# Kernel optimization log

Measured on AMD Instinct MI355X. Metric: run time of the kernel, lower is better.

The kernel has to match this reference:

```python
import jax, jax.numpy as jnp
import numpy as np

ALPHA = 0.95       # synaptic decay for layers l>0
BETA = 0.9         # membrane decay
THRESHOLD = 1.0
RESET = 0.0        # reset_potential
SIM_T = 100        # simulation_time
SG_SCALE = 100.0   # SuperSpike surrogate-gradient scale (SurrGradSpike)

@jax.custom_vjp
def spike(x):
    # forward: Heaviside step on (mem - threshold)
    return (x > 0).astype(x.dtype)

def _spike_fwd(x):
    return spike(x), x

def _spike_bwd(x, g):
    # SuperSpike surrogate: grad / (scale*|x| + 1)^2
    return (g / (SG_SCALE * jnp.abs(x) + 1.0) ** 2,)

spike.defvjp(_spike_fwd, _spike_bwd)


def setup_inputs() -> dict:
    key = jax.random.key(0)
    k1, k2, k3 = jax.random.split(key, 3)
    B, D, H = 256, 1024, 2048
    inputs = jax.random.normal(k1, (B, D), dtype=jnp.float32)
    w0 = jax.random.normal(k2, (D, H), dtype=jnp.float32) / np.sqrt(D).astype(np.float32)
    w1 = jax.random.normal(k3, (H, H), dtype=jnp.float32) / np.sqrt(H).astype(np.float32)
    return {"inputs": inputs, "w0": w0, "w1": w1}


def _simulate(inputs, w0, w1):
    B = inputs.shape[0]
    H0, H1 = w0.shape[1], w1.shape[1]
    # torch code does inputs.detach().clone() each step -> no grad to inputs
    x = jax.lax.stop_gradient(inputs)

    def step(carry, _):
        s0, m0, s1, m1 = carry
        # layer 0: new_syn = 0*syn + input @ W0
        ns0 = x @ w0
        nm0 = BETA * m0 + ns0
        mthr = nm0 - THRESHOLD          # hidden (non-final) layer spikes
        z = spike(mthr)
        nm0 = jnp.where(mthr > 0, RESET, nm0)   # masked reset after spike
        # layer 1 (final, non-spiking readout): new_syn = alpha*syn + z @ W1
        ns1 = ALPHA * s1 + z @ w1
        nm1 = BETA * m1 + ns1
        return (ns0, nm0, ns1, nm1), (nm0, nm1, z)

    init = (jnp.zeros((B, H0), jnp.float32), jnp.zeros((B, H0), jnp.float32),
            jnp.zeros((B, H1), jnp.float32), jnp.zeros((B, H1), jnp.float32))
    # torch loop records zeros at t==0 and updates for t=1..T-1
    _, (mem0_rec, mem1_rec, spk_rec) = jax.lax.scan(step, init, None, length=SIM_T - 1)
    z0 = jnp.zeros((1, B, H0), jnp.float32)
    z1 = jnp.zeros((1, B, H1), jnp.float32)
    mem0_rec = jnp.concatenate([z0, mem0_rec], axis=0)   # [T, B, H0]
    mem1_rec = jnp.concatenate([z1, mem1_rec], axis=0)   # [T, B, H1]
    spk_rec = jnp.concatenate([z0, spk_rec], axis=0)     # [T, B, H0]
    mem_rec = jnp.stack([mem0_rec, mem1_rec], axis=1)    # [T, L=2, B, H]
    return mem1_rec[-1], mem_rec, spk_rec


def reference(inputs, w0, w1):
    # returns (mem_rec[-1][-1], mem_rec, spk_rec) like the torch module
    return _simulate(inputs, w0, w1)
```

## Files before the change

### kernel.cpp

```cpp
#include <hip/hip_runtime.h>
#include <hip/hip_bf16.h>

#define Bdim 256
#define Ddim 1024
#define Hdim 2048
#define Tdim 100
#define BH (Bdim*Hdim)
#define M3 ((Tdim-1)*Bdim)
#define ZB8 ((size_t)M3*Hdim)

#define OUT_MEM ((size_t)BH)
#define OUT_SPK ((size_t)BH + (size_t)Tdim*2*BH)

typedef __attribute__((ext_vector_type(8))) short short8;
typedef __attribute__((ext_vector_type(4))) float f32x4;
typedef __attribute__((ext_vector_type(4))) int   i32x4;

#define GLD16(g, l) __builtin_amdgcn_global_load_lds( \
    (__attribute__((address_space(1))) void*)(g), \
    (__attribute__((address_space(3))) void*)(l), 16, 0, 0)

#define BARL() do { asm volatile("" ::: "memory"); __builtin_amdgcn_s_barrier(); \
                    asm volatile("" ::: "memory"); } while(0)

static __device__ __forceinline__ unsigned short bf16bits(float f) {
  __hip_bfloat16 h = __float2bfloat16(f);
  return *reinterpret_cast<unsigned short*>(&h);
}

__global__ __launch_bounds__(256) void kcvt_split(const float* __restrict__ X,
                                                  unsigned short* __restrict__ Xhi,
                                                  unsigned short* __restrict__ Xlo) {
  int i = (blockIdx.x*256 + threadIdx.x)*4;
  float4 v = *reinterpret_cast<const float4*>(&X[i]);
  ushort4 ph, pl;
  float f, fh;
  f = v.x; { __hip_bfloat16 h = __float2bfloat16(f); fh = __bfloat162float(h); ph.x = *reinterpret_cast<unsigned short*>(&h); } pl.x = bf16bits(f - fh);
  f = v.y; { __hip_bfloat16 h = __float2bfloat16(f); fh = __bfloat162float(h); ph.y = *reinterpret_cast<unsigned short*>(&h); } pl.y = bf16bits(f - fh);
  f = v.z; { __hip_bfloat16 h = __float2bfloat16(f); fh = __bfloat162float(h); ph.z = *reinterpret_cast<unsigned short*>(&h); } pl.z = bf16bits(f - fh);
  f = v.w; { __hip_bfloat16 h = __float2bfloat16(f); fh = __bfloat162float(h); ph.w = *reinterpret_cast<unsigned short*>(&h); } pl.w = bf16bits(f - fh);
  *reinterpret_cast<ushort4*>(&Xhi[i]) = ph;
  *reinterpret_cast<ushort4*>(&Xlo[i]) = pl;
}

__global__ __launch_bounds__(256) void ktr_split(const float* __restrict__ In,
                                                 unsigned short* __restrict__ OutHi,
                                                 unsigned short* __restrict__ OutLo,
                                                 int R, int C) {
  __shared__ unsigned short thi[32][33];
  __shared__ unsigned short tlo[32][33];
  int bk = blockIdx.x*32, bn = blockIdx.y*32;
  int tx = threadIdx.x & 31, ty = threadIdx.x >> 5;
  for (int r = ty; r < 32; r += 8) {
    float f = In[(size_t)(bk + r)*C + bn + tx];
    __hip_bfloat16 h = __float2bfloat16(f);
    float fh = __bfloat162float(h);
    thi[r][tx] = *reinterpret_cast<unsigned short*>(&h);
    tlo[r][tx] = bf16bits(f - fh);
  }
  __syncthreads();
  for (int r = ty; r < 32; r += 8) {
    OutHi[(size_t)(bn + r)*R + bk + tx] = thi[tx][r];
    OutLo[(size_t)(bn + r)*R + bk + tx] = tlo[tx][r];
  }
}

__global__ __launch_bounds__(256) void kcolmax_part(const float* __restrict__ W1,
                                                    float* __restrict__ pmax) {
  int n = blockIdx.x*256 + threadIdx.x;
  int kc = blockIdx.y;
  float m = 0.f;
  #pragma unroll 8
  for (int k = kc*64; k < kc*64 + 64; ++k)
    m = fmaxf(m, fabsf(W1[(size_t)k*Hdim + n]));
  pmax[(size_t)kc*Hdim + n] = m;
}

__global__ __launch_bounds__(256) void kcolmax_fin(const float* __restrict__ pmax,
                                                   float* __restrict__ scales) {
  int n = blockIdx.x*256 + threadIdx.x;
  float m = 0.f;
  #pragma unroll
  for (int i = 0; i < 32; ++i)
    m = fmaxf(m, pmax[(size_t)i*Hdim + n]);
  scales[n] = m * (1.0f/127.0f);
}

__global__ __launch_bounds__(256) void ktr_i8(const float* __restrict__ In,
                                              const float* __restrict__ scales,
                                              signed char* __restrict__ Out) {
  __shared__ signed char tile[32][33];
  int bk = blockIdx.x*32, bn = blockIdx.y*32;
  int tx = threadIdx.x & 31, ty = threadIdx.x >> 5;
  float rs = 1.0f / scales[bn + tx];
  for (int r = ty; r < 32; r += 8)
    tile[r][tx] = (signed char)(int)rintf(In[(size_t)(bk + r)*Hdim + bn + tx] * rs);
  __syncthreads();
  for (int r = ty; r < 32; r += 8)
    Out[(size_t)(bn + r)*Hdim + bk + tx] = tile[tx][r];
}

#define K1F_NK 32
__global__ __launch_bounds__(256) void k1_fused(const unsigned short* __restrict__ xhi,
                                                const unsigned short* __restrict__ xlo,
                                                const unsigned short* __restrict__ whiT,
                                                const unsigned short* __restrict__ wloT,
                                                float* __restrict__ NS0) {
  __shared__ short Ah[2][64*32], Al[2][64*32];
  __shared__ short Bh[2][64*32], Bl[2][64*32];
  int tid = threadIdx.x;
  int l = tid & 63, w = tid >> 6;
  int wm = w >> 1, wn = w & 1;
  int lr = l & 15, lg = l >> 4;
  size_t gm = (size_t)blockIdx.x * 64;
  size_t gn = (size_t)blockIdx.y * 64;
  int srow = l >> 2;
  int scol = ((l & 3)*8) ^ (((l >> 2) & 6) << 2);
  const unsigned short* gah = &xhi [(gm + w*16 + srow)*1024 + scol];
  const unsigned short* gal = &xlo [(gm + w*16 + srow)*1024 + scol];
  const unsigned short* gbh = &whiT[(gn + w*16 + srow)*1024 + scol];
  const unsigned short* gbl = &wloT[(gn + w*16 + srow)*1024 + scol];
  int rdswz = (lr & 6) << 2;
  f32x4 acc[2][2] = {};
  GLD16(gah, &Ah[0][w*512]); GLD16(gal, &Al[0][w*512]);
  GLD16(gbh, &Bh[0][w*512]); GLD16(gbl, &Bl[0][w*512]);
  __syncthreads();
  #pragma unroll 2
  for (int t = 0; t < K1F_NK; ++t) {
    int cur = t & 1;
    if (t + 1 < K1F_NK) {
      int nxt = cur ^ 1; size_t ko = (size_t)(t + 1)*32;
      GLD16(gah + ko, &Ah[nxt][w*512]); GLD16(gal + ko, &Al[nxt][w*512]);
      GLD16(gbh + ko, &Bh[nxt][w*512]); GLD16(gbl + ko, &Bl[nxt][w*512]);
    }
    short8 ah[2], al[2], bh[2], bl[2];
    #pragma unroll
    for (int mi = 0; mi < 2; ++mi) {
      int ro = (wm*32 + mi*16 + lr)*32 + (lg*8 ^ rdswz);
      ah[mi] = *reinterpret_cast<const short8*>(&Ah[cur][ro]);
      al[mi] = *reinterpret_cast<const short8*>(&Al[cur][ro]);
    }
    #pragma unroll
    for (int ni = 0; ni < 2; ++ni) {
      int ro = (wn*32 + ni*16 + lr)*32 + (lg*8 ^ rdswz);
      bh[ni] = *reinterpret_cast<const short8*>(&Bh[cur][ro]);
      bl[ni] = *reinterpret_cast<const short8*>(&Bl[cur][ro]);
    }
    #pragma unroll
    for (int mi = 0; mi < 2; ++mi)
      #pragma unroll
      for (int ni = 0; ni < 2; ++ni) {
        acc[mi][ni] = __builtin_amdgcn_mfma_f32_16x16x32_bf16(ah[mi], bh[ni], acc[mi][ni], 0, 0, 0);
        acc[mi][ni] = __builtin_amdgcn_mfma_f32_16x16x32_bf16(ah[mi], bl[ni], acc[mi][ni], 0, 0, 0);
        acc[mi][ni] = __builtin_amdgcn_mfma_f32_16x16x32_bf16(al[mi], bh[ni], acc[mi][ni], 0, 0, 0);
      }
    __syncthreads();
  }
  #pragma unroll
  for (int mi = 0; mi < 2; ++mi)
    #pragma unroll
    for (int ni = 0; ni < 2; ++ni)
      #pragma unroll
      for (int q = 0; q < 4; ++q)
        NS0[(gm + wm*32 + mi*16 + lg*4 + q)*Hdim + gn + wn*32 + ni*16 + lr] = acc[mi][ni][q];
}

__global__ __launch_bounds__(256) void k2_sim(const float* __restrict__ NS0,
                                              float* __restrict__ out,
                                              signed char* __restrict__ Zb) {
  size_t i4 = ((size_t)blockIdx.x*256 + threadIdx.x)*4;
  float4 nsv = *reinterpret_cast<const float4*>(&NS0[i4]);
  float ns[4] = {nsv.x, nsv.y, nsv.z, nsv.w};
  float* mem = out + OUT_MEM;
  float* spk = out + OUT_SPK;
  float4 z4 = {0.f, 0.f, 0.f, 0.f};
  *reinterpret_cast<float4*>(&mem[i4]) = z4;
  *reinterpret_cast<float4*>(&mem[BH + i4]) = z4;
  *reinterpret_cast<float4*>(&spk[i4]) = z4;
  float m[4] = {0.f, 0.f, 0.f, 0.f};
  for (int t = 1; t < Tdim; ++t) {
    float4 mo, zf; uchar4 z8;
    #pragma unroll
    for (int j = 0; j < 4; ++j) {
      m[j] = __fadd_rn(__fmul_rn(0.9f, m[j]), ns[j]);
      bool sp = m[j] > 1.0f;
      if (sp) m[j] = 0.f;
      ((float*)&mo)[j] = m[j];
      ((float*)&zf)[j] = sp ? 1.f : 0.f;
      ((unsigned char*)&z8)[j] = sp ? (unsigned char)1 : (unsigned char)0;
    }
    *reinterpret_cast<float4*>(&mem[(size_t)(2*t)*BH + i4]) = mo;
    *reinterpret_cast<float4*>(&spk[(size_t)t*BH + i4]) = zf;
    *reinterpret_cast<uchar4*>(&Zb[(size_t)(t-1)*BH + i4]) = z8;
  }
}

#define NKT3 32

#define K3_ST(g, ldsarr, half, kt) \
  GLD16((g) + (size_t)(kt)*64 + (size_t)(half)*128*2048, &ldsarr[(kt)&1][(half)*8192 + w*1024])

#define K3_LDA(h) do { \
  _Pragma("unroll") \
  for (int mi = 0; mi < 4; ++mi) \
    af[mi] = *reinterpret_cast<const i32x4*>( \
      &As[bb][((h)*128 + wm*64 + mi*16 + lr)*64 + ((lg ^ rxa)<<4)]); \
} while(0)

#define K3_LDB(v, bf) do { \
  _Pragma("unroll") \
  for (int ni = 0; ni < 2; ++ni) \
    bf[ni] = *reinterpret_cast<const i32x4*>( \
      &Bs[bb][((v)*128 + wn*32 + ni*16 + lr)*64 + ((lg ^ rxa)<<4)]); \
} while(0)

#define K3_MFMA(h, v, bf) do { \
  __builtin_amdgcn_s_setprio(1); \
  _Pragma("unroll") \
  for (int mi = 0; mi < 4; ++mi) \
    _Pragma("unroll") \
    for (int ni = 0; ni < 2; ++ni) \
      acc[(h)*4+mi][(v)*2+ni] = __builtin_amdgcn_mfma_i32_16x16x64_i8(af[mi], bf[ni], acc[(h)*4+mi][(v)*2+ni], 0, 0, 0); \
  __builtin_amdgcn_s_setprio(0); \
} while(0)

template<int CB>
__global__ __launch_bounds__(512, 2) void k3_gemm(const signed char* __restrict__ A,
                                                  const signed char* __restrict__ BT,
                                                  const float* __restrict__ scales,
                                                  float* __restrict__ mem1,
                                                  unsigned short* __restrict__ cbuf) {
  __shared__ signed char As[2][256*64];
  __shared__ signed char Bs[2][256*64];
  int tid = threadIdx.x;
  int l = tid & 63;
  int w = tid >> 6;
  int wm = w >> 2, wn = w & 3;
  int lr = l & 15, lg = l >> 4;
  int rxa = (lr >> 1) & 3;

  int lin = blockIdx.x;
  int wg = (lin & 7)*99 + (lin >> 3);
  int mtile = wg >> 3, ntile = wg & 7;
  size_t gm = (size_t)mtile * 256;
  size_t gn = (size_t)ntile * 256;

  int srow = l >> 2;
  int scol = ((l & 3) ^ ((l >> 3) & 3)) << 4;
  const signed char* gA = &A [(gm + w*16 + srow)*2048 + scol];
  const signed char* gB = &BT[(gn + w*16 + srow)*2048 + scol];

  i32x4 acc[8][4] = {};

  K3_ST(gA, As, 0, 0); K3_ST(gB, Bs, 0, 0);
  K3_ST(gA, As, 1, 0); K3_ST(gB, Bs, 1, 0);
  K3_ST(gA, As, 0, 1); K3_ST(gB, Bs, 1, 1);

  for (int kt = 0; kt < NKT3; ++kt) {
    int bb = kt & 1;
    if (kt == NKT3 - 1) asm volatile("s_waitcnt vmcnt(0)" ::: "memory");
    else                asm volatile("s_waitcnt vmcnt(2)" ::: "memory");
    __builtin_amdgcn_s_barrier();
    asm volatile("" ::: "memory");

    i32x4 af[4], bfl[2], bfh[2];

    K3_LDA(0); K3_LDB(0, bfl);
    if (kt + 1 < NKT3) K3_ST(gA, As, 1, kt + 1);
    BARL();
    K3_MFMA(0, 0, bfl);
    BARL();
    K3_LDB(1, bfh);
    if (kt + 1 < NKT3) K3_ST(gB, Bs, 0, kt + 1);
    BARL();
    K3_MFMA(0, 1, bfh);
    BARL();
    K3_LDA(1);
    if (kt + 2 < NKT3) K3_ST(gA, As, 0, kt + 2);
    BARL();
    K3_MFMA(1, 1, bfh);
    BARL();
    if (kt + 2 < NKT3) K3_ST(gB, Bs, 1, kt + 2);
    K3_MFMA(1, 0, bfl);
  }

  float sc[2][2];
  #pragma unroll
  for (int vv = 0; vv < 2; ++vv)
    #pragma unroll
    for (int ni = 0; ni < 2; ++ni)
      sc[vv][ni] = scales[gn + vv*128 + wn*32 + ni*16 + lr];

  if (CB) {
    unsigned short* cp = cbuf + (size_t)mtile*BH + gn;
    #pragma unroll
    for (int hh = 0; hh < 2; ++hh)
      #pragma unroll
      for (int mi = 0; mi < 4; ++mi)
        #pragma unroll
        for (int vv = 0; vv < 2; ++vv)
          #pragma unroll
          for (int ni = 0; ni < 2; ++ni)
            #pragma unroll
            for (int q = 0; q < 4; ++q) {
              int b   = hh*128 + wm*64 + mi*16 + lg*4 + q;
              int col = vv*128 + wn*32 + ni*16 + lr;
              cp[(size_t)b*Hdim + col] =
                bf16bits((float)acc[hh*4+mi][vv*2+ni][q] * sc[vv][ni]);
            }
  } else {
    float* plane = mem1 + (size_t)(2*mtile + 3)*BH + gn;
    #pragma unroll
    for (int hh = 0; hh < 2; ++hh)
      #pragma unroll
      for (int mi = 0; mi < 4; ++mi)
        #pragma unroll
        for (int vv = 0; vv < 2; ++vv)
          #pragma unroll
          for (int ni = 0; ni < 2; ++ni)
            #pragma unroll
            for (int q = 0; q < 4; ++q) {
              int b   = hh*128 + wm*64 + mi*16 + lg*4 + q;
              int col = vv*128 + wn*32 + ni*16 + lr;
              plane[(size_t)b*Hdim + col] =
                (float)acc[hh*4+mi][vv*2+ni][q] * sc[vv][ni];
            }
  }
}

__global__ __launch_bounds__(256) void k4_rec(float* __restrict__ out) {
  size_t i4 = ((size_t)blockIdx.x*256 + threadIdx.x)*4;
  float* mem = out + OUT_MEM;
  float s[4] = {0.f,0.f,0.f,0.f}, m[4] = {0.f,0.f,0.f,0.f};
  for (int t = 1; t < Tdim; ++t) {
    float4* p = reinterpret_cast<float4*>(&mem[(size_t)(2*t + 1)*BH + i4]);
    float4 c = *p;
    float4 mo;
    #pragma unroll
    for (int j = 0; j < 4; ++j) {
      s[j] = __fadd_rn(__fmul_rn(0.95f, s[j]), ((float*)&c)[j]);
      m[j] = __fadd_rn(__fmul_rn(0.9f, m[j]), s[j]);
      ((float*)&mo)[j] = m[j];
    }
    *p = mo;
  }
  float4 o = {m[0], m[1], m[2], m[3]};
  *reinterpret_cast<float4*>(&out[i4]) = o;
}

__global__ __launch_bounds__(256) void k4_rec_cb(const unsigned short* __restrict__ C,
                                                 float* __restrict__ out) {
  size_t i4 = ((size_t)blockIdx.x*256 + threadIdx.x)*4;
  float* mem = out + OUT_MEM;
  float s[4] = {0.f,0.f,0.f,0.f}, m[4] = {0.f,0.f,0.f,0.f};
  for (int t = 1; t < Tdim; ++t) {
    ushort4 cv = *reinterpret_cast<const ushort4*>(&C[(size_t)(t-1)*BH + i4]);
    float4 mo;
    #pragma unroll
    for (int j = 0; j < 4; ++j) {
      unsigned int u = ((unsigned short*)&cv)[j];
      float c = __uint_as_float(u << 16);
      s[j] = __fadd_rn(__fmul_rn(0.95f, s[j]), c);
      m[j] = __fadd_rn(__fmul_rn(0.9f, m[j]), s[j]);
      ((float*)&mo)[j] = m[j];
    }
    *reinterpret_cast<float4*>(&mem[(size_t)(2*t + 1)*BH + i4]) = mo;
  }
  float4 o = {m[0], m[1], m[2], m[3]};
  *reinterpret_cast<float4*>(&out[i4]) = o;
}

extern "C" void kernel_launch(void* const* d_in, const int* in_sizes, int n_in,
                              void* d_out, int out_size, void* d_ws, size_t ws_size,
                              hipStream_t stream) {
  const float* X  = (const float*)d_in[0];
  const float* W0 = (const float*)d_in[1];
  const float* W1 = (const float*)d_in[2];
  float* out = (float*)d_out;
  char* ws = (char*)d_ws;

  float*          ns0    = (float*)ws;
  signed char*    w1t8   = (signed char*)(ws + (2ull << 20));
  float*          scales = (float*)(ws + (6ull << 20));
  float*          pmax   = (float*)(ws + (6ull << 20) + (64ull << 10));
  signed char*    zb     = (signed char*)(ws + (10ull << 20));
  unsigned short* cbuf   = (unsigned short*)(ws + (10ull << 20) + ZB8);
  size_t needCb = (10ull << 20) + ZB8 + (size_t)M3*Hdim*2;
  int useCb = (ws_size >= needCb) ? 1 : 0;
  unsigned short* xhi = (unsigned short*)(ws + (10ull << 20));
  unsigned short* xlo = (unsigned short*)(ws + (10ull << 20) + (512<<10));
  unsigned short* whi = (unsigned short*)(ws + (11ull << 20));
  unsigned short* wlo = (unsigned short*)(ws + (15ull << 20));

  kcvt_split  <<<dim3(256),     256, 0, stream>>>(X, xhi, xlo);
  ktr_split   <<<dim3(32, 64),  256, 0, stream>>>(W0, whi, wlo, 1024, 2048);
  kcolmax_part<<<dim3(8, 32),   256, 0, stream>>>(W1, pmax);
  kcolmax_fin <<<dim3(8),       256, 0, stream>>>(pmax, scales);
  ktr_i8      <<<dim3(64, 64),  256, 0, stream>>>(W1, scales, w1t8);
  k1_fused    <<<dim3(4, 32),   256, 0, stream>>>(xhi, xlo, whi, wlo, ns0);
  k2_sim      <<<dim3(BH/1024), 256, 0, stream>>>(ns0, out, zb);
  if (useCb) {
    k3_gemm<1><<<dim3((M3/256)*(Hdim/256)), 512, 0, stream>>>(zb, w1t8, scales, out + OUT_MEM, cbuf);
    k4_rec_cb<<<dim3(BH/1024), 256, 0, stream>>>(cbuf, out);
  } else {
    k3_gemm<0><<<dim3((M3/256)*(Hdim/256)), 512, 0, stream>>>(zb, w1t8, scales, out + OUT_MEM, cbuf);
    k4_rec  <<<dim3(BH/1024), 256, 0, stream>>>(out);
  }
}
```

Baseline: 377.2 us.

## Simplify int8 GEMM main loop to whole-tile double buffering with one barrier

Replaces the staggered half-tile prefetch schedule in the int8 GEMM, which put a barrier around each MFMA quarter, with a plain double-buffered loop. Each iteration now issues all global-to-LDS loads for the next K tile, runs the four MFMA groups on the current tile, then waits for the loads and synchronises once. This cuts barrier count and scheduling constraints per K step. In exchange, loads are issued only one tile ahead and are drained fully before every barrier, so memory latency may be hidden less well.

```diff
diff --git a/kernel.cpp b/kernel.cpp
--- a/kernel.cpp
+++ b/kernel.cpp
@@ -19,9 +19,6 @@
 #define GLD16(g, l) __builtin_amdgcn_global_load_lds( \
     (__attribute__((address_space(1))) void*)(g), \
     (__attribute__((address_space(3))) void*)(l), 16, 0, 0)
-
-#define BARL() do { asm volatile("" ::: "memory"); __builtin_amdgcn_s_barrier(); \
-                    asm volatile("" ::: "memory"); } while(0)
 
 static __device__ __forceinline__ unsigned short bf16bits(float f) {
   __hip_bfloat16 h = __float2bfloat16(f);
@@ -252,36 +249,28 @@
 
   i32x4 acc[8][4] = {};
 
-  K3_ST(gA, As, 0, 0); K3_ST(gB, Bs, 0, 0);
-  K3_ST(gA, As, 1, 0); K3_ST(gB, Bs, 1, 0);
-  K3_ST(gA, As, 0, 1); K3_ST(gB, Bs, 1, 1);
+  K3_ST(gA, As, 0, 0); K3_ST(gA, As, 1, 0);
+  K3_ST(gB, Bs, 0, 0); K3_ST(gB, Bs, 1, 0);
+  asm volatile("s_waitcnt vmcnt(0)" ::: "memory");
+  __builtin_amdgcn_s_barrier();
+  asm volatile("" ::: "memory");
 
   for (int kt = 0; kt < NKT3; ++kt) {
     int bb = kt & 1;
-    if (kt == NKT3 - 1) asm volatile("s_waitcnt vmcnt(0)" ::: "memory");
-    else                asm volatile("s_waitcnt vmcnt(2)" ::: "memory");
+    if (kt + 1 < NKT3) {
+      K3_ST(gA, As, 0, kt + 1); K3_ST(gA, As, 1, kt + 1);
+      K3_ST(gB, Bs, 0, kt + 1); K3_ST(gB, Bs, 1, kt + 1);
+    }
+    i32x4 af[4], bfl[2], bfh[2];
+    K3_LDA(0); K3_LDB(0, bfl); K3_LDB(1, bfh);
+    K3_MFMA(0, 0, bfl);
+    K3_MFMA(0, 1, bfh);
+    K3_LDA(1);
+    K3_MFMA(1, 0, bfl);
+    K3_MFMA(1, 1, bfh);
+    asm volatile("s_waitcnt vmcnt(0)" ::: "memory");
     __builtin_amdgcn_s_barrier();
     asm volatile("" ::: "memory");
-
-    i32x4 af[4], bfl[2], bfh[2];
-
-    K3_LDA(0); K3_LDB(0, bfl);
-    if (kt + 1 < NKT3) K3_ST(gA, As, 1, kt + 1);
-    BARL();
-    K3_MFMA(0, 0, bfl);
-    BARL();
-    K3_LDB(1, bfh);
-    if (kt + 1 < NKT3) K3_ST(gB, Bs, 0, kt + 1);
-    BARL();
-    K3_MFMA(0, 1, bfh);
-    BARL();
-    K3_LDA(1);
-    if (kt + 2 < NKT3) K3_ST(gA, As, 0, kt + 2);
-    BARL();
-    K3_MFMA(1, 1, bfh);
-    BARL();
-    if (kt + 2 < NKT3) K3_ST(gB, Bs, 1, kt + 2);
-    K3_MFMA(1, 0, bfl);
   }
 
   float sc[2][2];
```

Result: slower. 403.2 us (+6.9%).
